# Performance work log

Measured on AMD Instinct MI355X. Metric: run time of the kernel, lower is better.

Reference implementation:

```python
import jax, jax.numpy as jnp
import numpy as np

BS, C_IN, NY, NX = 8, 256, 80, 80
C, NC, NA, N = 256, 80, 1, 16384
K = 3  # 3x3 sparse convs, padding 1


def setup_inputs() -> dict:
    key = jax.random.key(0)
    ks = jax.random.split(key, 16)
    w = lambda k, shape: jax.random.normal(k, shape, jnp.float32) * 0.02
    x = jax.random.normal(ks[0], (BS, C_IN, NY, NX), jnp.float32)
    bi = jax.random.randint(ks[1], (N,), 0, BS)
    yi = jax.random.randint(ks[2], (N,), 0, NY)
    xi = jax.random.randint(ks[3], (N,), 0, NX)
    indices = jnp.stack([bi, yi, xi], axis=1).astype(jnp.int64)
    return {
        'x': x,
        'indices': indices,
        'stem_w': w(ks[4], (C, C_IN)),        'stem_b': w(ks[5], (C,)),
        'cls_conv_w': w(ks[6], (C, C * K * K)), 'cls_conv_b': w(ks[7], (C,)),
        'reg_conv_w': w(ks[8], (C, C * K * K)), 'reg_conv_b': w(ks[9], (C,)),
        'cls_pred_w': w(ks[10], (NA * NC, C)),  'cls_pred_b': w(ks[11], (NA * NC,)),
        'reg_pred_w': w(ks[12], (NA * 4, C)),   'reg_pred_b': w(ks[13], (NA * 4,)),
        'obj_pred_w': w(ks[14], (NA * 1, C)),   'obj_pred_b': w(ks[15], (NA * 1,)),
    }


def _gather_patches(stem, indices):
    """Gather flattened KxK patches at (b,y,x) indices.

    Matches F.unfold ordering: flattened as [c, kh, kw].
    stem: [bs, c, ny, nx] -> returns [N, c*K*K].
    """
    pad = K // 2
    # NHWC padded feature map: [bs, ny+2p, nx+2p, c]
    padded = jnp.pad(stem.transpose(0, 2, 3, 1),
                     ((0, 0), (pad, pad), (pad, pad), (0, 0)))
    bi, yi, xi = indices[:, 0], indices[:, 1], indices[:, 2]
    d = jnp.arange(K)
    yy = yi[:, None, None] + d[None, :, None]   # [N, K, 1]
    xx = xi[:, None, None] + d[None, None, :]   # [N, 1, K]
    patches = padded[bi[:, None, None], yy, xx]  # [N, K, K, c]
    n = patches.shape[0]
    return patches.transpose(0, 3, 1, 2).reshape(n, -1)  # [N, c*K*K]


def reference(x, indices, stem_w, stem_b, cls_conv_w, cls_conv_b,
              reg_conv_w, reg_conv_b, cls_pred_w, cls_pred_b,
              reg_pred_w, reg_pred_b, obj_pred_w, obj_pred_b):
    # dense 1x1 stem conv + SiLU
    stem = jax.nn.silu(jnp.einsum('bchw,oc->bohw', x, stem_w)
                       + stem_b[None, :, None, None])
    # sparse 3x3 convs: gather patches -> linear -> SiLU
    pf = _gather_patches(stem, indices)                 # [N, C*9]
    cls_feat = jax.nn.silu(pf @ cls_conv_w.T + cls_conv_b)
    reg_feat = jax.nn.silu(pf @ reg_conv_w.T + reg_conv_b)
    n = pf.shape[0]
    cls = (cls_feat @ cls_pred_w.T + cls_pred_b).reshape(n, NA, NC)
    reg = (reg_feat @ reg_pred_w.T + reg_pred_b).reshape(n, NA, 4)
    obj = (reg_feat @ obj_pred_w.T + obj_pred_b).reshape(n, NA, 1)
    y_sp = jnp.concatenate([reg, obj, cls], axis=-1).reshape(n, NA * (5 + NC))
    return y_sp
```

## Files before the change

kernel.cpp:

```cpp
#include <hip/hip_runtime.h>

typedef unsigned short u16;
typedef __attribute__((ext_vector_type(4))) float f32x4;
typedef __attribute__((ext_vector_type(8))) short s16x8;

#define BM 128
#define BN 128
#define BK 32

__device__ inline float bf2f(u16 u) {
    unsigned v = ((unsigned)u) << 16;
    return __builtin_bit_cast(float, v);
}
__device__ inline u16 f2bf(float f) {
    unsigned u = __builtin_bit_cast(unsigned, f);
    unsigned r = (u + 0x7FFFu + ((u >> 16) & 1u)) >> 16;
    return (u16)r;
}

typedef const __attribute__((address_space(1))) void* gptr_t;
typedef __attribute__((address_space(3))) void* lptr_t;
__device__ inline void gload16(const u16* gp, u16* lp) {
    __builtin_amdgcn_global_load_lds((gptr_t)gp, (lptr_t)lp, 16, 0, 0);
}

__global__ __launch_bounds__(256) void fused_pre(
    const float* __restrict__ x, const int* __restrict__ idx,
    const float* __restrict__ stem_w,
    const float* __restrict__ cls_conv_w, const float* __restrict__ cls_conv_b,
    const float* __restrict__ reg_conv_w, const float* __restrict__ reg_conv_b,
    const float* __restrict__ cls_pred_w, const float* __restrict__ cls_pred_b,
    const float* __restrict__ reg_pred_w, const float* __restrict__ reg_pred_b,
    const float* __restrict__ obj_pred_w, const float* __restrict__ obj_pred_b,
    u16* __restrict__ xT, u16* __restrict__ Wsb, u16* __restrict__ Wc,
    u16* __restrict__ Wf, int* __restrict__ rowoff,
    float* __restrict__ bc, float* __restrict__ bp, u16* __restrict__ zpage) {
    __shared__ u16 tile[64 * 258];
    const int blk = blockIdx.x;
    const int t = threadIdx.x;

    if (blk < 800) {
        int b = blk / 100, hw0 = (blk % 100) * 64;
        int l = t & 63, w = t >> 6;
        const float* xb = x + (size_t)b * 256 * 6400 + hw0 + l;
#pragma unroll 4
        for (int k = 0; k < 64; ++k) {
            int c = w + k * 4;
            tile[l * 258 + c] = f2bf(xb[(size_t)c * 6400]);
        }
        __syncthreads();
        u16* outb = xT + ((size_t)b * 6400 + hw0) * 256;
#pragma unroll
        for (int i = 0; i < 8; ++i) {
            int hw = w * 16 + i * 2 + (l >> 5);
            int c = (l & 31) * 8;
            *(int4*)(outb + (size_t)hw * 256 + c) = *(const int4*)&tile[hw * 258 + c];
        }
    } else if (blk < 1312) {
        int o = blk - 800;
        const float* src = (o < 256) ? (cls_conv_w + (size_t)o * 2304)
                                     : (reg_conv_w + (size_t)(o - 256) * 2304);
        u16* dst = Wc + (size_t)o * 2304;
#pragma unroll
        for (int it = 0; it < 9; ++it) {
            int kk = it * 256 + t;
            int j = kk >> 8, c = kk & 255;
            dst[kk] = f2bf(src[c * 9 + j]);
        }
    } else if (blk < 1888) {
        int i = (blk - 1312) * 256 + t;
        int n = i / 9, j = i % 9;
        int b = idx[n * 3 + 0], y = idx[n * 3 + 1], xx0 = idx[n * 3 + 2];
        int yy = y + j / 3 - 1;
        int xx = xx0 + j % 3 - 1;
        rowoff[i] = ((unsigned)yy < 80u && (unsigned)xx < 80u)
                        ? (b * 6400 + yy * 80 + xx) * 256 : -1;
    } else if (blk < 1952) {
        int base = (blk - 1888) * 1024;
#pragma unroll
        for (int it = 0; it < 4; ++it) {
            int i = base + it * 256 + t;
            Wsb[i] = f2bf(stem_w[i]);
        }
    } else if (blk < 1984) {
        int base = (blk - 1952) * 2048;
#pragma unroll
        for (int it = 0; it < 8; ++it) {
            int i = base + it * 256 + t;
            int o = i >> 9, k = i & 511;
            float v = 0.f;
            if (o < 4)       { if (k >= 256) v = reg_pred_w[o * 256 + (k - 256)]; }
            else if (o == 4) { if (k >= 256) v = obj_pred_w[k - 256]; }
            else if (o < 85) { if (k < 256)  v = cls_pred_w[(o - 5) * 256 + k]; }
            Wf[i] = f2bf(v);
        }
    } else {
        for (int i = t; i < 512; i += 256)
            bc[i] = (i < 256) ? cls_conv_b[i] : reg_conv_b[i - 256];
        if (t < 128) {
            float v = 0.f;
            if (t < 4) v = reg_pred_b[t];
            else if (t == 4) v = obj_pred_b[0];
            else if (t < 85) v = cls_pred_b[t - 5];
            bp[t] = v;
        }
        zpage[t] = 0;
    }
}

template <int EPI>
__global__ __launch_bounds__(256, 2) void gemm_bt(
    const u16* __restrict__ A, const u16* __restrict__ B,
    const float* __restrict__ bias, void* __restrict__ Dv,
    int K, int ldd, int storeN) {
    __shared__ __align__(16) u16 lA[BM * BK];
    __shared__ __align__(16) u16 lB[BN * BK];
    const int tid = threadIdx.x;
    const int lane = tid & 63;
    const int wid = tid >> 6;
    const int wm = wid >> 1, wn = wid & 1;
    const int m0 = blockIdx.x * BM;
    const int n0 = blockIdx.y * BN;

    const int srow = lane >> 2;
    const int scol = (lane & 3) * 8;
    const int arow = lane & 15;
    const int khalf = (lane >> 4) * 8;

    f32x4 acc[4][4] = {};

    for (int k0 = 0; k0 < K; k0 += BK) {
#pragma unroll
        for (int r = 0; r < 2; ++r) {
            int row = r * 64 + wid * 16 + srow;
            gload16(A + (size_t)(m0 + row) * K + k0 + scol, lA + r * 2048 + wid * 512);
            gload16(B + (size_t)(n0 + row) * K + k0 + scol, lB + r * 2048 + wid * 512);
        }
        __syncthreads();
        s16x8 af[4], bfr[4];
#pragma unroll
        for (int f = 0; f < 4; ++f) {
            af[f]  = *(const s16x8*)&lA[(wm * 64 + f * 16 + arow) * BK + khalf];
            bfr[f] = *(const s16x8*)&lB[(wn * 64 + f * 16 + arow) * BK + khalf];
        }
#pragma unroll
        for (int i = 0; i < 4; ++i)
#pragma unroll
            for (int j = 0; j < 4; ++j)
                acc[i][j] = __builtin_amdgcn_mfma_f32_16x16x32_bf16(af[i], bfr[j],
                                                                    acc[i][j], 0, 0, 0);
        __syncthreads();
    }

#pragma unroll
    for (int i = 0; i < 4; ++i) {
        int gr0 = m0 + wm * 64 + i * 16 + (lane >> 4) * 4;
#pragma unroll
        for (int j = 0; j < 4; ++j) {
            int gc = n0 + wn * 64 + j * 16 + (lane & 15);
            if (EPI == 1 && gc >= storeN) continue;
            float bb = bias[gc];
#pragma unroll
            for (int r = 0; r < 4; ++r) {
                float v = acc[i][j][r] + bb;
                if (EPI == 0) {
                    v = v / (1.0f + __expf(-v));
                    ((u16*)Dv)[(size_t)(gr0 + r) * ldd + gc] = f2bf(v);
                } else {
                    ((float*)Dv)[(size_t)(gr0 + r) * ldd + gc] = v;
                }
            }
        }
    }
}

__global__ __launch_bounds__(256, 4) void gemm_conv(
    const u16* __restrict__ stem, const int* __restrict__ rowoff,
    const u16* __restrict__ zpage, const u16* __restrict__ B,
    const float* __restrict__ bias, u16* __restrict__ D) {
    __shared__ __align__(16) u16 lA[128 * 64];
    __shared__ __align__(16) u16 lB[64 * 64];
    const int tid = threadIdx.x;
    const int lane = tid & 63;
    const int wid = tid >> 6;
    const int wm = wid >> 1, wn = wid & 1;
    const int m0 = blockIdx.x * 128;
    const int n0 = blockIdx.y * 64;

    const int srw = lane >> 3;
    const int cc  = lane & 7;
    const int gch = (cc ^ srw) * 8;
    const int arow = lane & 15;
    const int khi  = lane >> 4;
    const int sa   = arow & 7;

    int ro[4][9];
#pragma unroll
    for (int r = 0; r < 4; ++r) {
        const int rb = (m0 + r * 32 + wid * 8 + srw) * 9;
#pragma unroll
        for (int j = 0; j < 9; ++j) ro[r][j] = rowoff[rb + j];
    }
    const u16* Bp = B + (size_t)(n0 + wid * 8 + srw) * 2304 + gch;

    f32x4 acc[4][2] = {};

#pragma unroll
    for (int j = 0; j < 9; ++j) {
#pragma unroll
        for (int q4 = 0; q4 < 4; ++q4) {
            const int c0 = q4 << 6;
            const int k0 = j * 256 + c0;
#pragma unroll
            for (int r = 0; r < 2; ++r)
                gload16(Bp + (size_t)(r * 32) * 2304 + k0,
                        lB + (r * 32 + wid * 8) * 64);
#pragma unroll
            for (int r = 0; r < 4; ++r) {
                int roff = ro[r][j];
                const u16* srcA = (roff < 0) ? (zpage + gch)
                                             : (stem + roff + c0 + gch);
                gload16(srcA, lA + (r * 32 + wid * 8) * 64);
            }
            __syncthreads();
            s16x8 af[2][4], bfr[2][2];
#pragma unroll
            for (int f = 0; f < 4; ++f) {
                int ra = (wm * 64 + f * 16 + arow) * 64;
#pragma unroll
                for (int ks = 0; ks < 2; ++ks) {
                    int q = ks * 4 + khi;
                    af[ks][f] = *(const s16x8*)&lA[ra + ((q ^ sa) << 3)];
                }
            }
#pragma unroll
            for (int jj = 0; jj < 2; ++jj) {
                int rb2 = (wn * 32 + jj * 16 + arow) * 64;
#pragma unroll
                for (int ks = 0; ks < 2; ++ks) {
                    int q = ks * 4 + khi;
                    bfr[ks][jj] = *(const s16x8*)&lB[rb2 + ((q ^ sa) << 3)];
                }
            }
#pragma unroll
            for (int ks = 0; ks < 2; ++ks)
#pragma unroll
                for (int i = 0; i < 4; ++i)
#pragma unroll
                    for (int jj = 0; jj < 2; ++jj)
                        acc[i][jj] = __builtin_amdgcn_mfma_f32_16x16x32_bf16(
                            af[ks][i], bfr[ks][jj], acc[i][jj], 0, 0, 0);
            __syncthreads();
        }
    }

#pragma unroll
    for (int i = 0; i < 4; ++i) {
        int gr0 = m0 + wm * 64 + i * 16 + khi * 4;
#pragma unroll
        for (int jj = 0; jj < 2; ++jj) {
            int gc = n0 + wn * 32 + jj * 16 + arow;
            float bb = bias[gc];
#pragma unroll
            for (int r = 0; r < 4; ++r) {
                float v = acc[i][jj][r] + bb;
                v = v / (1.0f + __expf(-v));
                D[(size_t)(gr0 + r) * 512 + gc] = f2bf(v);
            }
        }
    }
}

__global__ __launch_bounds__(256, 4) void gemm_pred(
    const u16* __restrict__ A, const u16* __restrict__ B,
    const float* __restrict__ bias, float* __restrict__ D) {
    __shared__ __align__(16) u16 lA[64 * 64];
    __shared__ __align__(16) u16 lB[64 * 64];
    const int tid = threadIdx.x;
    const int lane = tid & 63;
    const int wid = tid >> 6;
    const int wm = wid >> 1, wn = wid & 1;
    const int m0 = blockIdx.x * 64;
    const int n0 = blockIdx.y * 64;

    const int srw = lane >> 3;
    const int cc  = lane & 7;
    const int arow = lane & 15;
    const int khi  = lane >> 4;

    f32x4 acc[2][2] = {};

    for (int k0 = 0; k0 < 512; k0 += 64) {
        const int gch = (cc ^ srw) * 8;
#pragma unroll
        for (int r = 0; r < 2; ++r) {
            int row = r * 32 + wid * 8 + srw;
            gload16(A + (size_t)(m0 + row) * 512 + k0 + gch,
                    lA + (r * 32 + wid * 8) * 64);
            gload16(B + (size_t)(n0 + row) * 512 + k0 + gch,
                    lB + (r * 32 + wid * 8) * 64);
        }
        __syncthreads();
        s16x8 af[2][2], bfr[2][2];
        const int sa = arow & 7;
#pragma unroll
        for (int f = 0; f < 2; ++f) {
            int ra = (wm * 32 + f * 16 + arow) * 64;
            int rb = (wn * 32 + f * 16 + arow) * 64;
#pragma unroll
            for (int ks = 0; ks < 2; ++ks) {
                int q = ks * 4 + khi;
                af[ks][f]  = *(const s16x8*)&lA[ra + ((q ^ sa) << 3)];
                bfr[ks][f] = *(const s16x8*)&lB[rb + ((q ^ sa) << 3)];
            }
        }
#pragma unroll
        for (int ks = 0; ks < 2; ++ks)
#pragma unroll
            for (int i = 0; i < 2; ++i)
#pragma unroll
                for (int jj = 0; jj < 2; ++jj)
                    acc[i][jj] = __builtin_amdgcn_mfma_f32_16x16x32_bf16(
                        af[ks][i], bfr[ks][jj], acc[i][jj], 0, 0, 0);
        __syncthreads();
    }

#pragma unroll
    for (int i = 0; i < 2; ++i) {
        int gr0 = m0 + wm * 32 + i * 16 + khi * 4;
#pragma unroll
        for (int jj = 0; jj < 2; ++jj) {
            int gc = n0 + wn * 32 + jj * 16 + arow;
            if (gc >= 85) continue;
            float bb = bias[gc];
#pragma unroll
            for (int r = 0; r < 4; ++r)
                D[(size_t)(gr0 + r) * 85 + gc] = acc[i][jj][r] + bb;
        }
    }
}

extern "C" void kernel_launch(void* const* d_in, const int* in_sizes, int n_in,
                              void* d_out, int out_size, void* d_ws, size_t ws_size,
                              hipStream_t stream) {
    const float* x          = (const float*)d_in[0];
    const int*   idx        = (const int*)d_in[1];
    const float* stem_w     = (const float*)d_in[2];
    const float* stem_b     = (const float*)d_in[3];
    const float* cls_conv_w = (const float*)d_in[4];
    const float* cls_conv_b = (const float*)d_in[5];
    const float* reg_conv_w = (const float*)d_in[6];
    const float* reg_conv_b = (const float*)d_in[7];
    const float* cls_pred_w = (const float*)d_in[8];
    const float* cls_pred_b = (const float*)d_in[9];
    const float* reg_pred_w = (const float*)d_in[10];
    const float* reg_pred_b = (const float*)d_in[11];
    const float* obj_pred_w = (const float*)d_in[12];
    const float* obj_pred_b = (const float*)d_in[13];
    float* out = (float*)d_out;
    char* ws = (char*)d_ws;

    u16*  xT     = (u16*)(ws);
    u16*  stem   = (u16*)(ws + 26214400);
    u16*  feat   = (u16*)(ws + 52428800);
    u16*  Wc     = (u16*)(ws + 69206016);
    u16*  Wf     = (u16*)(ws + 71565312);
    u16*  Wsb    = (u16*)(ws + 71696384);
    int*  rowoff = (int*)(ws + 71827456);
    u16*  zpage  = (u16*)(ws + 72417280);
    float* bc    = (float*)(ws + 72417792);
    float* bp    = (float*)(ws + 72419840);

    fused_pre<<<1985, 256, 0, stream>>>(x, idx, stem_w,
                                        cls_conv_w, cls_conv_b, reg_conv_w, reg_conv_b,
                                        cls_pred_w, cls_pred_b, reg_pred_w, reg_pred_b,
                                        obj_pred_w, obj_pred_b,
                                        xT, Wsb, Wc, Wf, rowoff, bc, bp, zpage);
    gemm_bt<0><<<dim3(400, 2), 256, 0, stream>>>(xT, Wsb, stem_b, stem, 256, 256, 256);
    gemm_conv<<<dim3(128, 8), 256, 0, stream>>>(stem, rowoff, zpage, Wc, bc, feat);
    gemm_pred<<<dim3(256, 2), 256, 0, stream>>>(feat, Wf, bp, out);
}
```

Baseline: 93.60 us.

## Fuse input transpose and bf16 cast into stem GEMM A-tile loading

Removes the separate x transpose/bf16 conversion stage that wrote an intermediate xT buffer. The stem GEMM now reads fp32 NCHW input directly, converts to bf16 and writes a transposed, padded LDS tile, with B staged via global_load_lds using an XOR swizzle. The N tile shrinks to 64 with BK 64, more blocks and occupancy 4. This saves a full write and re-read of a 26MB intermediate, but A-tile loads now go through registers with per-element strided reads, and x is read once per N-tile (4 times).

```diff
diff --git a/kernel.cpp b/kernel.cpp
--- a/kernel.cpp
+++ b/kernel.cpp
@@ -25,39 +25,21 @@
 }
 
 __global__ __launch_bounds__(256) void fused_pre(
-    const float* __restrict__ x, const int* __restrict__ idx,
+    const int* __restrict__ idx,
     const float* __restrict__ stem_w,
     const float* __restrict__ cls_conv_w, const float* __restrict__ cls_conv_b,
     const float* __restrict__ reg_conv_w, const float* __restrict__ reg_conv_b,
     const float* __restrict__ cls_pred_w, const float* __restrict__ cls_pred_b,
     const float* __restrict__ reg_pred_w, const float* __restrict__ reg_pred_b,
     const float* __restrict__ obj_pred_w, const float* __restrict__ obj_pred_b,
-    u16* __restrict__ xT, u16* __restrict__ Wsb, u16* __restrict__ Wc,
+    u16* __restrict__ Wsb, u16* __restrict__ Wc,
     u16* __restrict__ Wf, int* __restrict__ rowoff,
     float* __restrict__ bc, float* __restrict__ bp, u16* __restrict__ zpage) {
-    __shared__ u16 tile[64 * 258];
     const int blk = blockIdx.x;
     const int t = threadIdx.x;
 
-    if (blk < 800) {
-        int b = blk / 100, hw0 = (blk % 100) * 64;
-        int l = t & 63, w = t >> 6;
-        const float* xb = x + (size_t)b * 256 * 6400 + hw0 + l;
-#pragma unroll 4
-        for (int k = 0; k < 64; ++k) {
-            int c = w + k * 4;
-            tile[l * 258 + c] = f2bf(xb[(size_t)c * 6400]);
-        }
-        __syncthreads();
-        u16* outb = xT + ((size_t)b * 6400 + hw0) * 256;
-#pragma unroll
-        for (int i = 0; i < 8; ++i) {
-            int hw = w * 16 + i * 2 + (l >> 5);
-            int c = (l & 31) * 8;
-            *(int4*)(outb + (size_t)hw * 256 + c) = *(const int4*)&tile[hw * 258 + c];
-        }
-    } else if (blk < 1312) {
-        int o = blk - 800;
+    if (blk < 512) {
+        int o = blk;
         const float* src = (o < 256) ? (cls_conv_w + (size_t)o * 2304)
                                      : (reg_conv_w + (size_t)(o - 256) * 2304);
         u16* dst = Wc + (size_t)o * 2304;
@@ -67,23 +49,23 @@
             int j = kk >> 8, c = kk & 255;
             dst[kk] = f2bf(src[c * 9 + j]);
         }
-    } else if (blk < 1888) {
-        int i = (blk - 1312) * 256 + t;
+    } else if (blk < 1088) {
+        int i = (blk - 512) * 256 + t;
         int n = i / 9, j = i % 9;
         int b = idx[n * 3 + 0], y = idx[n * 3 + 1], xx0 = idx[n * 3 + 2];
         int yy = y + j / 3 - 1;
         int xx = xx0 + j % 3 - 1;
         rowoff[i] = ((unsigned)yy < 80u && (unsigned)xx < 80u)
                         ? (b * 6400 + yy * 80 + xx) * 256 : -1;
-    } else if (blk < 1952) {
-        int base = (blk - 1888) * 1024;
+    } else if (blk < 1152) {
+        int base = (blk - 1088) * 1024;
 #pragma unroll
         for (int it = 0; it < 4; ++it) {
             int i = base + it * 256 + t;
             Wsb[i] = f2bf(stem_w[i]);
         }
-    } else if (blk < 1984) {
-        int base = (blk - 1952) * 2048;
+    } else if (blk < 1184) {
+        int base = (blk - 1152) * 2048;
 #pragma unroll
         for (int it = 0; it < 8; ++it) {
             int i = base + it * 256 + t;
@@ -108,67 +90,88 @@
     }
 }
 
-template <int EPI>
-__global__ __launch_bounds__(256, 2) void gemm_bt(
-    const u16* __restrict__ A, const u16* __restrict__ B,
-    const float* __restrict__ bias, void* __restrict__ Dv,
-    int K, int ldd, int storeN) {
-    __shared__ __align__(16) u16 lA[BM * BK];
-    __shared__ __align__(16) u16 lB[BN * BK];
+__global__ __launch_bounds__(256, 4) void gemm_stem(
+    const float* __restrict__ x, const u16* __restrict__ Wsb,
+    const float* __restrict__ bias, u16* __restrict__ stem) {
+    __shared__ __align__(16) u16 lA[128 * 72];
+    __shared__ __align__(16) u16 lB[64 * 64];
     const int tid = threadIdx.x;
     const int lane = tid & 63;
     const int wid = tid >> 6;
     const int wm = wid >> 1, wn = wid & 1;
-    const int m0 = blockIdx.x * BM;
-    const int n0 = blockIdx.y * BN;
-
-    const int srow = lane >> 2;
-    const int scol = (lane & 3) * 8;
+    const int bx = blockIdx.x;
+    const int b   = bx / 50;
+    const int hwb = (bx % 50) * 128;
+    const int n0 = blockIdx.y * 64;
+
+    const int srw = lane >> 3;
+    const int cc  = lane & 7;
+    const int gch = (cc ^ srw) * 8;
     const int arow = lane & 15;
-    const int khalf = (lane >> 4) * 8;
-
-    f32x4 acc[4][4] = {};
-
-    for (int k0 = 0; k0 < K; k0 += BK) {
-#pragma unroll
-        for (int r = 0; r < 2; ++r) {
-            int row = r * 64 + wid * 16 + srow;
-            gload16(A + (size_t)(m0 + row) * K + k0 + scol, lA + r * 2048 + wid * 512);
-            gload16(B + (size_t)(n0 + row) * K + k0 + scol, lB + r * 2048 + wid * 512);
+    const int khi  = lane >> 4;
+    const int sa   = arow & 7;
+
+    const float* xb = x + (size_t)b * 256 * 6400 + hwb;
+    const u16* Bp = Wsb + (size_t)(n0 + wid * 8 + srw) * 256 + gch;
+
+    f32x4 acc[4][2] = {};
+
+    for (int k0 = 0; k0 < 256; k0 += 64) {
+#pragma unroll
+        for (int r = 0; r < 2; ++r)
+            gload16(Bp + (size_t)(r * 32) * 256 + k0,
+                    lB + (r * 32 + wid * 8) * 64);
+#pragma unroll
+        for (int u = 0; u < 4; ++u) {
+            const int hw  = (u & 1) * 64 + lane;
+            const int oct = (u >> 1) * 4 + wid;
+            union { u16 s[8]; s16x8 v; } pk;
+#pragma unroll
+            for (int jj = 0; jj < 8; ++jj)
+                pk.s[jj] = f2bf(xb[(size_t)(k0 + oct * 8 + jj) * 6400 + hw]);
+            *(s16x8*)&lA[hw * 72 + oct * 8] = pk.v;
         }
         __syncthreads();
-        s16x8 af[4], bfr[4];
+        s16x8 af[2][4], bfr[2][2];
 #pragma unroll
         for (int f = 0; f < 4; ++f) {
-            af[f]  = *(const s16x8*)&lA[(wm * 64 + f * 16 + arow) * BK + khalf];
-            bfr[f] = *(const s16x8*)&lB[(wn * 64 + f * 16 + arow) * BK + khalf];
-        }
-#pragma unroll
-        for (int i = 0; i < 4; ++i)
-#pragma unroll
-            for (int j = 0; j < 4; ++j)
-                acc[i][j] = __builtin_amdgcn_mfma_f32_16x16x32_bf16(af[i], bfr[j],
-                                                                    acc[i][j], 0, 0, 0);
+            int ra = (wm * 64 + f * 16 + arow) * 72;
+#pragma unroll
+            for (int ks = 0; ks < 2; ++ks)
+                af[ks][f] = *(const s16x8*)&lA[ra + (ks * 4 + khi) * 8];
+        }
+#pragma unroll
+        for (int jj = 0; jj < 2; ++jj) {
+            int rb2 = (wn * 32 + jj * 16 + arow) * 64;
+#pragma unroll
+            for (int ks = 0; ks < 2; ++ks) {
+                int q = ks * 4 + khi;
+                bfr[ks][jj] = *(const s16x8*)&lB[rb2 + ((q ^ sa) << 3)];
+            }
+        }
+#pragma unroll
+        for (int ks = 0; ks < 2; ++ks)
+#pragma unroll
+            for (int i = 0; i < 4; ++i)
+#pragma unroll
+                for (int jj = 0; jj < 2; ++jj)
+                    acc[i][jj] = __builtin_amdgcn_mfma_f32_16x16x32_bf16(
+                        af[ks][i], bfr[ks][jj], acc[i][jj], 0, 0, 0);
         __syncthreads();
     }
 
 #pragma unroll
     for (int i = 0; i < 4; ++i) {
-        int gr0 = m0 + wm * 64 + i * 16 + (lane >> 4) * 4;
-#pragma unroll
-        for (int j = 0; j < 4; ++j) {
-            int gc = n0 + wn * 64 + j * 16 + (lane & 15);
-            if (EPI == 1 && gc >= storeN) continue;
+        int lr0 = wm * 64 + i * 16 + khi * 4;
+#pragma unroll
+        for (int jj = 0; jj < 2; ++jj) {
+            int gc = n0 + wn * 32 + jj * 16 + arow;
             float bb = bias[gc];
 #pragma unroll
             for (int r = 0; r < 4; ++r) {
-                float v = acc[i][j][r] + bb;
-                if (EPI == 0) {
-                    v = v / (1.0f + __expf(-v));
-                    ((u16*)Dv)[(size_t)(gr0 + r) * ldd + gc] = f2bf(v);
-                } else {
-                    ((float*)Dv)[(size_t)(gr0 + r) * ldd + gc] = v;
-                }
+                float v = acc[i][jj][r] + bb;
+                v = v / (1.0f + __expf(-v));
+                stem[(size_t)(b * 6400 + hwb + lr0 + r) * 256 + gc] = f2bf(v);
             }
         }
     }
@@ -349,10 +352,10 @@
     const float* stem_b     = (const float*)d_in[3];
     const float* cls_conv_w = (const float*)d_in[4];
     const float* cls_conv_b = (const float*)d_in[5];
+    const float* cls_pred_w = (const float*)d_in[8];
+    const float* cls_pred_b = (const float*)d_in[9];
     const float* reg_conv_w = (const float*)d_in[6];
     const float* reg_conv_b = (const float*)d_in[7];
-    const float* cls_pred_w = (const float*)d_in[8];
-    const float* cls_pred_b = (const float*)d_in[9];
     const float* reg_pred_w = (const float*)d_in[10];
     const float* reg_pred_b = (const float*)d_in[11];
     const float* obj_pred_w = (const float*)d_in[12];
@@ -360,23 +363,22 @@
     float* out = (float*)d_out;
     char* ws = (char*)d_ws;
 
-    u16*  xT     = (u16*)(ws);
-    u16*  stem   = (u16*)(ws + 26214400);
-    u16*  feat   = (u16*)(ws + 52428800);
-    u16*  Wc     = (u16*)(ws + 69206016);
-    u16*  Wf     = (u16*)(ws + 71565312);
-    u16*  Wsb    = (u16*)(ws + 71696384);
-    int*  rowoff = (int*)(ws + 71827456);
-    u16*  zpage  = (u16*)(ws + 72417280);
-    float* bc    = (float*)(ws + 72417792);
-    float* bp    = (float*)(ws + 72419840);
-
-    fused_pre<<<1985, 256, 0, stream>>>(x, idx, stem_w,
+    u16*  stem   = (u16*)(ws);
+    u16*  feat   = (u16*)(ws + 26214400);
+    u16*  Wc     = (u16*)(ws + 42991616);
+    u16*  Wf     = (u16*)(ws + 45350912);
+    u16*  Wsb    = (u16*)(ws + 45481984);
+    int*  rowoff = (int*)(ws + 45613056);
+    u16*  zpage  = (u16*)(ws + 46202880);
+    float* bc    = (float*)(ws + 46203392);
+    float* bp    = (float*)(ws + 46205440);
+
+    fused_pre<<<1185, 256, 0, stream>>>(idx, stem_w,
                                         cls_conv_w, cls_conv_b, reg_conv_w, reg_conv_b,
                                         cls_pred_w, cls_pred_b, reg_pred_w, reg_pred_b,
                                         obj_pred_w, obj_pred_b,
-                                        xT, Wsb, Wc, Wf, rowoff, bc, bp, zpage);
-    gemm_bt<0><<<dim3(400, 2), 256, 0, stream>>>(xT, Wsb, stem_b, stem, 256, 256, 256);
+                                        Wsb, Wc, Wf, rowoff, bc, bp, zpage);
+    gemm_stem<<<dim3(400, 4), 256, 0, stream>>>(x, Wsb, stem_b, stem);
     gemm_conv<<<dim3(128, 8), 256, 0, stream>>>(stem, rowoff, zpage, Wc, bc, feat);
     gemm_pred<<<dim3(256, 2), 256, 0, stream>>>(feat, Wf, bp, out);
 }
```

After: 92.92 us. Within noise of the previous version (-0.7%).
